# Optimization experiments

Hardware: AMD Instinct MI355X
Metric: run time of the kernel (lower is better)

Reference implementation:

```python
import math
import jax, jax.numpy as jnp
import numpy as np


def fwht(x):
    """Fast Walsh-Hadamard transform along the last axis (natural/Hadamard order).

    x: (..., n) with n a power of two. O(n log n) butterfly, fully vectorized
    over all leading dims.
    """
    lead = x.shape[:-1]
    n = x.shape[-1]
    m = int(math.log2(n))
    assert 1 << m == n, "FWHT requires power-of-two length"
    x = x.reshape(-1, n)
    h = 2
    for _ in range(m):
        # view rows as blocks of size h; butterfly combine halves of each block
        xb = x.reshape(-1, n // h, h)
        a = xb[..., : h // 2]
        b = xb[..., h // 2 :]
        x = jnp.concatenate([a + b, a - b], axis=-1).reshape(-1, n)
        h *= 2
    return x.reshape(lead + (n,))


def setup_inputs() -> dict:
    key = jax.random.key(0)
    x = jax.random.normal(key, (2, 8192, 4096), dtype=jnp.float32)
    return {"x": x}


def reference(x) -> jnp.ndarray:
    # Power-of-two path of InverseHadamardTransform: normalized FWHT.
    # (had_K is None, K == 1 for out_features = 4096.)
    n = x.shape[-1]
    scale = 1.0 / math.sqrt(n)
    return fwht(x) * jnp.asarray(scale, dtype=x.dtype)
```

## Files before the change

### kernel.cpp

```cpp
#include <hip/hip_runtime.h>


__device__ __forceinline__ void fwht16(float v[16]) {
#pragma unroll
    for (int s = 1; s < 16; s <<= 1) {
#pragma unroll
        for (int i = 0; i < 16; ++i) {
            if ((i & s) == 0) {
                float a = v[i];
                float b = v[i | s];
                v[i]     = a + b;
                v[i | s] = a - b;
            }
        }
    }
}

__global__ __launch_bounds__(256) void fwht4096_kernel(const float* __restrict__ x,
                                                       float* __restrict__ out) {
    __shared__ float lds[4352];

    const int t = threadIdx.x;
    const size_t base = (size_t)blockIdx.x * 4096;

    float v[16];

    const float4* px4 = (const float4*)(x + base);
#pragma unroll
    for (int k = 0; k < 4; ++k) {
        float4 q = px4[t * 4 + k];
        v[4 * k + 0] = q.x;
        v[4 * k + 1] = q.y;
        v[4 * k + 2] = q.z;
        v[4 * k + 3] = q.w;
    }

    fwht16(v);

#pragma unroll
    for (int j = 0; j < 16; ++j) lds[17 * t + j] = v[j];
    __syncthreads();

    {
        const int t_lo = t & 15, t_hi = t >> 4;
        const int b1 = t_lo + 272 * t_hi;
#pragma unroll
        for (int j = 0; j < 16; ++j) v[j] = lds[b1 + 17 * j];
    }

    fwht16(v);
    __syncthreads();

    {
        const int t_lo = t & 15, t_hi = t >> 4;
        const int b2 = t_lo + 272 * t_hi;
#pragma unroll
        for (int j = 0; j < 16; ++j) lds[b2 + 16 * j] = v[j];
    }
    __syncthreads();

#pragma unroll
    for (int j = 0; j < 16; ++j) v[j] = lds[t + 272 * j];

    fwht16(v);

    const float scale = 0.015625f;
    float* po = out + base;
#pragma unroll
    for (int j = 0; j < 16; ++j) po[t + 256 * j] = v[j] * scale;
}

extern "C" void kernel_launch(void* const* d_in, const int* in_sizes, int n_in,
                              void* d_out, int out_size, void* d_ws, size_t ws_size,
                              hipStream_t stream) {
    const float* x = (const float*)d_in[0];
    float* out = (float*)d_out;
    const int rows = in_sizes[0] >> 12;
    fwht4096_kernel<<<rows, 256, 0, stream>>>(x, out);
}
```

Measured before the change: 424.3 us.

## Restructure FWHT data layout for coalesced float4 global I/O and LDS transposes

```diff
diff --git a/kernel.cpp b/kernel.cpp
--- a/kernel.cpp
+++ b/kernel.cpp
@@ -7,8 +7,7 @@
 #pragma unroll
         for (int i = 0; i < 16; ++i) {
             if ((i & s) == 0) {
-                float a = v[i];
-                float b = v[i | s];
+                float a = v[i], b = v[i | s];
                 v[i]     = a + b;
                 v[i | s] = a - b;
             }
@@ -18,56 +17,79 @@
 
 __global__ __launch_bounds__(256) void fwht4096_kernel(const float* __restrict__ x,
                                                        float* __restrict__ out) {
-    __shared__ float lds[4352];
+    __shared__ float lds[5120];
 
     const int t = threadIdx.x;
     const size_t base = (size_t)blockIdx.x * 4096;
-
     float v[16];
 
-    const float4* px4 = (const float4*)(x + base);
+    const float4* px = (const float4*)(x + base);
 #pragma unroll
     for (int k = 0; k < 4; ++k) {
-        float4 q = px4[t * 4 + k];
-        v[4 * k + 0] = q.x;
-        v[4 * k + 1] = q.y;
-        v[4 * k + 2] = q.z;
-        v[4 * k + 3] = q.w;
+        float4 q = px[t + 256 * k];
+        v[4*k+0] = q.x; v[4*k+1] = q.y; v[4*k+2] = q.z; v[4*k+3] = q.w;
     }
 
     fwht16(v);
 
+    {
+        const int gw = t + (t >> 4);
 #pragma unroll
-    for (int j = 0; j < 16; ++j) lds[17 * t + j] = v[j];
+        for (int k = 0; k < 4; ++k) {
+            *(float4*)&lds[4 * (gw + 274 * k)] =
+                make_float4(v[4*k], v[4*k+1], v[4*k+2], v[4*k+3]);
+        }
+    }
     __syncthreads();
 
     {
-        const int t_lo = t & 15, t_hi = t >> 4;
-        const int b1 = t_lo + 272 * t_hi;
+        const int rb = 4 * (17 * (t >> 4) + 274 * ((t >> 2) & 3)) + (t & 3);
 #pragma unroll
-        for (int j = 0; j < 16; ++j) v[j] = lds[b1 + 17 * j];
+        for (int j = 0; j < 16; ++j) v[j] = lds[rb + 4 * j];
+    }
+
+    fwht16(v);
+    __syncthreads();
+
+#pragma unroll
+    for (int k = 0; k < 4; ++k) {
+        *(float4*)&lds[20 * t + 4 * k] =
+            make_float4(v[4*k], v[4*k+1], v[4*k+2], v[4*k+3]);
+    }
+    __syncthreads();
+
+    {
+        const int rb = 20 * (t & 15) + (t >> 4);
+#pragma unroll
+        for (int j = 0; j < 16; ++j) v[j] = lds[rb + 320 * j];
     }
 
     fwht16(v);
     __syncthreads();
 
     {
-        const int t_lo = t & 15, t_hi = t >> 4;
-        const int b2 = t_lo + 272 * t_hi;
+        const int wb = 4 * ((t >> 4) + 274 * ((t >> 2) & 3)) + (t & 3);
 #pragma unroll
-        for (int j = 0; j < 16; ++j) lds[b2 + 16 * j] = v[j];
+        for (int j = 0; j < 16; ++j) lds[wb + 68 * j] = v[j];
     }
     __syncthreads();
 
+    {
+        const int gw = t + (t >> 4);
 #pragma unroll
-    for (int j = 0; j < 16; ++j) v[j] = lds[t + 272 * j];
-
-    fwht16(v);
+        for (int k = 0; k < 4; ++k) {
+            float4 q = *(const float4*)&lds[4 * (gw + 274 * k)];
+            v[4*k+0] = q.x; v[4*k+1] = q.y; v[4*k+2] = q.z; v[4*k+3] = q.w;
+        }
+    }
 
     const float scale = 0.015625f;
-    float* po = out + base;
+    float4* po = (float4*)(out + base);
 #pragma unroll
-    for (int j = 0; j < 16; ++j) po[t + 256 * j] = v[j] * scale;
+    for (int k = 0; k < 4; ++k) {
+        po[t + 256 * k] = make_float4(v[4*k] * scale, v[4*k+1] * scale,
+                                      v[4*k+2] * scale, v[4*k+3] * scale);
+    }
 }
 
 extern "C" void kernel_launch(void* const* d_in, const int* in_sizes, int n_in,
```

New measurement: 425.8 us. Within noise of the previous version (+0.4%).
